# Optimization experiments

Hardware: AMD Instinct MI355X
Metric: run time of the kernel (lower is better)

## Reference

```python
import jax, jax.numpy as jnp
import numpy as np

DIM, HEADS = 768, 12
HEAD_DIM = DIM // HEADS
SCALE = HEAD_DIM ** -0.5


def setup_inputs() -> dict:
    key = jax.random.key(0)
    ks = jax.random.split(key, 16)
    B, LQ, LK = 8, 512, 512
    s = DIM ** -0.5
    inp = {
        "query": jax.random.normal(ks[0], (B, LQ, DIM), jnp.float32),
        "key_value": jax.random.normal(ks[1], (B, LK, DIM), jnp.float32),
        "query_coords": jax.random.normal(ks[2], (LQ, 2), jnp.float32),
        "key_coords": jax.random.normal(ks[3], (LK, 2), jnp.float32),
        "Wq": jax.random.normal(ks[4], (DIM, DIM), jnp.float32) * s,
        "bq": jnp.zeros((DIM,), jnp.float32),
        "Wk": jax.random.normal(ks[5], (DIM, DIM), jnp.float32) * s,
        "bk": jnp.zeros((DIM,), jnp.float32),
        "Wv": jax.random.normal(ks[6], (DIM, DIM), jnp.float32) * s,
        "bv": jnp.zeros((DIM,), jnp.float32),
        "Wo": jax.random.normal(ks[7], (DIM, DIM), jnp.float32) * s,
        "bo": jnp.zeros((DIM,), jnp.float32),
        "W1": jax.random.normal(ks[8], (6, DIM), jnp.float32) * (6 ** -0.5),
        "b1": jnp.zeros((DIM,), jnp.float32),
        "W2": jax.random.normal(ks[9], (DIM, HEADS), jnp.float32) * s,
        "b2": jnp.zeros((HEADS,), jnp.float32),
    }
    return inp


def reference(query, key_value, query_coords, key_coords,
              Wq, bq, Wk, bk, Wv, bv, Wo, bo, W1, b1, W2, b2):
    B, LQ, _ = query.shape
    LK = key_value.shape[1]
    # QKV projections -> [B, L, H, Dh]
    q = (query @ Wq + bq).reshape(B, LQ, HEADS, HEAD_DIM)
    k = (key_value @ Wk + bk).reshape(B, LK, HEADS, HEAD_DIM)
    v = (key_value @ Wv + bv).reshape(B, LK, HEADS, HEAD_DIM)
    # attention logits [B, H, LQ, LK]
    logits = jnp.einsum('bqhd,bkhd->bhqk', q, k) * SCALE
    # pairwise relative bias: delta [LQ, LK, 2] -> rel [LQ, LK, 6]
    delta = query_coords[:, None, :] - key_coords[None, :, :]
    rel = jnp.concatenate([delta, jnp.abs(delta), jnp.square(delta)], axis=-1)
    hidden = jax.nn.gelu(rel @ W1 + b1, approximate=False)  # [LQ, LK, DIM]
    bias = hidden @ W2 + b2  # [LQ, LK, H]
    logits = logits + jnp.transpose(bias, (2, 0, 1))[None]  # [B,H,LQ,LK]
    weights = jax.nn.softmax(logits, axis=-1)
    out = jnp.einsum('bhqk,bkhd->bqhd', weights, v).reshape(B, LQ, DIM)
    return out @ Wo + bo
```

## Files before the change

### kernel.cpp

```cpp
#include <hip/hip_runtime.h>
#include <hip/hip_bf16.h>
#include <stdint.h>
#include <math.h>

typedef __attribute__((ext_vector_type(4))) float f32x4;
typedef _Float16 f16;
typedef __attribute__((ext_vector_type(8))) _Float16 f16x8;
typedef decltype(__builtin_amdgcn_cvt_pkrtz(0.f, 0.f)) pk16;

#define DIM   768
#define NH    12
#define HD    64
#define NB    8
#define SEQ   512
#define SCALE 0.125f

#define GN    161
#define GPTS  (GN * GN)

#define MFMA16H __builtin_amdgcn_mfma_f32_16x16x32_f16

struct PrepArgs {
    const float* query; const float* key_value; f16* Xq; f16* Xkv;
    const float* W[4]; f16* WT[4];
    const float* W1; const float* b1; const float* W2;
    f16* W1tab; f16* W2tab; float* gtab32;
};

__global__ void __launch_bounds__(256) k_prep(PrepArgs pa) {
    __shared__ float tt[32][33];
    int g = blockIdx.x, t = threadIdx.x;
    if (g < 3072) {
        const float* in = (g < 1536) ? pa.query : pa.key_value;
        f16* out = (g < 1536) ? pa.Xq : pa.Xkv;
        int i = (g % 1536) * 256 + t;
        const float4* s = reinterpret_cast<const float4*>(in + i * 8);
        float4 f0 = s[0], f1 = s[1];
        union { pk16 h[4]; uint4 v; } o;
        o.h[0] = __builtin_amdgcn_cvt_pkrtz(f0.x, f0.y);
        o.h[1] = __builtin_amdgcn_cvt_pkrtz(f0.z, f0.w);
        o.h[2] = __builtin_amdgcn_cvt_pkrtz(f1.x, f1.y);
        o.h[3] = __builtin_amdgcn_cvt_pkrtz(f1.z, f1.w);
        reinterpret_cast<uint4*>(out)[i] = o.v;
    } else if (g < 5376) {
        int bi = g - 3072;
        int z = bi / 576, rem = bi % 576;
        int bx = rem % 24, by = rem / 24;
        const float* W = pa.W[z];
        f16* WT = pa.WT[z];
        int n0 = bx * 32, k0 = by * 32;
        int tx = t & 31, ty = t >> 5;
#pragma unroll
        for (int j = 0; j < 4; ++j)
            tt[ty + 8 * j][tx] = W[(k0 + ty + 8 * j) * DIM + n0 + tx];
        __syncthreads();
#pragma unroll
        for (int j = 0; j < 4; ++j)
            WT[(n0 + ty + 8 * j) * DIM + k0 + tx] = (f16)tt[tx][ty + 8 * j];
    } else {
        int i = (g - 5376) * 256 + t;
        if (i < 3072) {
            int lane = i & 63;
            int hi = lane >> 4, m = lane & 15;
            int u = (i >> 6) * 16 + m;
#pragma unroll
            for (int e = 0; e < 8; ++e) {
                float v = 0.f;
                if (hi == 0) {
                    if (e < 6) v = pa.W1[e * DIM + u];
                    else if (e == 6) v = pa.b1[u];
                }
                pa.W1tab[i * 8 + e] = (f16)v;
            }
        } else if (i < 4608) {
            int i2 = i - 3072;
            int j = i2 >> 6, lane = i2 & 63;
            int gq = lane >> 4, h = lane & 15;
#pragma unroll
            for (int e = 0; e < 8; ++e) {
                int u = 32 * j + ((e >> 2) << 4) + (gq << 2) + (e & 3);
                float v = (h < 12) ? pa.W2[u * 12 + h] : 0.f;
                pa.W2tab[i2 * 8 + e] = (f16)v;
            }
        } else {
            int i2 = i - 4608;
            float x = (i2 + 0.5f) * (1.0f / 256.0f) - 8.0f;
            pa.gtab32[i2] = 0.5f * x * (1.0f + erff(x * 0.70710678f));
        }
    }
}

__global__ void __launch_bounds__(256) k_grid(const f16x8* __restrict__ W1tab,
                                              const f16x8* __restrict__ W2tab,
                                              const float* __restrict__ b2,
                                              const float* __restrict__ gtab32,
                                              f16* __restrict__ grid16) {
    __shared__ float tab[4096];
    int t = threadIdx.x, lane = t & 63, w = t >> 6;
    {
        const uint4* gt = (const uint4*)gtab32;
        uint4* st = (uint4*)tab;
#pragma unroll
        for (int i = 0; i < 4; ++i) st[i * 256 + t] = gt[i * 256 + t];
    }
    int hi = lane >> 4, m = lane & 15;
    int p0 = blockIdx.x * 64 + w * 16;
    int p = p0 + m;
    int gy = p / GN, gx = p - gy * GN;
    float dx = gx * 0.125f - 10.0f;
    float dy = gy * 0.125f - 10.0f;

    union { f16x8 v; pk16 h2[4]; } rf;
    { f16x8 zz = {}; rf.v = zz; }
    if (hi == 0) {
        rf.h2[0] = __builtin_amdgcn_cvt_pkrtz(dx, dy);
        rf.h2[1] = __builtin_amdgcn_cvt_pkrtz(fabsf(dx), fabsf(dy));
        rf.h2[2] = __builtin_amdgcn_cvt_pkrtz(dx * dx, dy * dy);
        rf.h2[3] = __builtin_amdgcn_cvt_pkrtz(1.0f, 0.0f);
    }

    float b2h = (m < 12) ? b2[m] : 0.f;
    f32x4 acc = {b2h, b2h, b2h, b2h};
    const f32x4 zero = {};
    const f16x8* w1p = W1tab + lane;
    const f16x8* w2p = W2tab + lane;
    __syncthreads();

#pragma unroll 2
    for (int j = 0; j < 24; ++j) {
        f16x8 a0  = w1p[(2 * j) * 64];
        f16x8 a1  = w1p[(2 * j + 1) * 64];
        f16x8 w2v = w2p[j * 64];
        f32x4 pre0 = MFMA16H(a0, rf.v, zero, 0, 0, 0);
        f32x4 pre1 = MFMA16H(a1, rf.v, zero, 0, 0, 0);
        float s0[4], s1[4];
#pragma unroll
        for (int e = 0; e < 4; ++e) {
            float x0 = pre0[e];
            float xi0 = __builtin_amdgcn_fmed3f(__builtin_fmaf(x0, 256.f, 2048.f), 0.f, 4095.f);
            float g0 = tab[(int)xi0];
            s0[e] = (x0 > 8.f) ? x0 : g0;
            float x1 = pre1[e];
            float xi1 = __builtin_amdgcn_fmed3f(__builtin_fmaf(x1, 256.f, 2048.f), 0.f, 4095.f);
            float g1 = tab[(int)xi1];
            s1[e] = (x1 > 8.f) ? x1 : g1;
        }
        union { f16x8 v; pk16 h2[4]; } pav;
        pav.h2[0] = __builtin_amdgcn_cvt_pkrtz(s0[0], s0[1]);
        pav.h2[1] = __builtin_amdgcn_cvt_pkrtz(s0[2], s0[3]);
        pav.h2[2] = __builtin_amdgcn_cvt_pkrtz(s1[0], s1[1]);
        pav.h2[3] = __builtin_amdgcn_cvt_pkrtz(s1[2], s1[3]);
        acc = MFMA16H(pav.v, w2v, acc, 0, 0, 0);
    }
    if (m < 12) {
#pragma unroll
        for (int r = 0; r < 4; ++r) {
            int pr = p0 + hi * 4 + r;
            if (pr < GPTS) grid16[pr * 16 + m] = (f16)acc[r];
        }
    }
}

struct MQArgs {
    const float* qc; const float* kc;
    const f16* grid16; f16* bias16;
    const f16* Xq; const f16* Xkv;
    const f16* WqT; const f16* WkT; const f16* WvT;
    const float* bq; const float* bk; const float* bv;
    f16* q_ws; f16* k_ws; f16* v_t;
};

__global__ void __launch_bounds__(256) k_mq5(MQArgs a) {
    __shared__ uint4 lds[1024];
    int bid = blockIdx.x, t = threadIdx.x;
    int lane = t & 63, w = t >> 6;
    int hi = lane >> 4, lm = lane & 15;
    int xcd = bid & 7, slot = bid >> 3;

    if (slot >= 16) {
        int lid = xcd * 288 + (slot - 16);
        int m_group = lid / 36;
        int within = lid - m_group * 36;
        int z = within / 12;
        int n_tile = within - z * 12;
        int m0 = m_group * 64, n0 = n_tile * 64;
        const f16* X = (z == 0) ? a.Xq : a.Xkv;
        const f16* Wt = (z == 0) ? a.WqT : (z == 1) ? a.WkT : a.WvT;
        const float* bias = (z == 0) ? a.bq : (z == 1) ? a.bk : a.bv;
        f16* out = (z == 0) ? a.q_ws : (z == 1) ? a.k_ws : a.v_t;

        int wr = w >> 1, wc = w & 1;
        int srow = t >> 2, sslot = t & 3;
        const f16* Ag = X + (m0 + srow) * DIM + sslot * 8;
        const f16* Bg = Wt + (n0 + srow) * DIM + sslot * 8;
        int wi = srow * 4 + (sslot ^ ((srow >> 1) & 3));

        int aidx[2], bidx[2];
#pragma unroll
        for (int i = 0; i < 2; ++i) {
            int ar = wr * 32 + i * 16 + lm;
            aidx[i] = ar * 4 + (hi ^ ((ar >> 1) & 3));
            int br = wc * 32 + i * 16 + lm;
            bidx[i] = 256 + br * 4 + (hi ^ ((br >> 1) & 3));
        }

        f32x4 acc[2][2] = {};
        {
            uint4 a0 = *(const uint4*)(Ag);
            uint4 b0 = *(const uint4*)(Bg);
            lds[wi] = a0;
            lds[256 + wi] = b0;
        }
        uint4 sA1 = *(const uint4*)(Ag + 32);
        uint4 sB1 = *(const uint4*)(Bg + 32);
        uint4 sA0 = *(const uint4*)(Ag + 64);
        uint4 sB0 = *(const uint4*)(Bg + 64);
        __syncthreads();

#define MQ_COMPUTE(kt)                                                        \
        {                                                                     \
            int bo = ((kt) & 1) << 9;                                         \
            f16x8 af0 = *(const f16x8*)&lds[bo + aidx[0]];                    \
            f16x8 af1 = *(const f16x8*)&lds[bo + aidx[1]];                    \
            f16x8 bf0 = *(const f16x8*)&lds[bo + bidx[0]];                    \
            f16x8 bf1 = *(const f16x8*)&lds[bo + bidx[1]];                    \
            acc[0][0] = MFMA16H(af0, bf0, acc[0][0], 0, 0, 0);                \
            acc[0][1] = MFMA16H(af0, bf1, acc[0][1], 0, 0, 0);                \
            acc[1][0] = MFMA16H(af1, bf0, acc[1][0], 0, 0, 0);                \
            acc[1][1] = MFMA16H(af1, bf1, acc[1][1], 0, 0, 0);                \
        }

        for (int kp = 0; kp < 12; ++kp) {
            int kt = 2 * kp;
            MQ_COMPUTE(kt)
            {
                int bo2 = (((kt) & 1) << 9) ^ 512;
                lds[bo2 + wi] = sA1;
                lds[bo2 + 256 + wi] = sB1;
                if (kt + 3 < 24) {
                    sA1 = *(const uint4*)(Ag + (kt + 3) * 32);
                    sB1 = *(const uint4*)(Bg + (kt + 3) * 32);
                }
                __syncthreads();
            }
            kt = 2 * kp + 1;
            MQ_COMPUTE(kt)
            if (kt < 23) {
                int bo2 = (((kt) & 1) << 9) ^ 512;
                lds[bo2 + wi] = sA0;
                lds[bo2 + 256 + wi] = sB0;
                if (kt + 3 < 24) {
                    sA0 = *(const uint4*)(Ag + (kt + 3) * 32);
                    sB0 = *(const uint4*)(Bg + (kt + 3) * 32);
                }
                __syncthreads();
            }
        }
#undef MQ_COMPUTE

#pragma unroll
        for (int mi = 0; mi < 2; ++mi)
#pragma unroll
            for (int ni = 0; ni < 2; ++ni) {
                int n = n0 + wc * 32 + ni * 16 + lm;
                float bn = bias[n];
                int h = n >> 6, d = n & 63;
                int mbase = m0 + wr * 32 + mi * 16 + hi * 4;
                int bb = mbase >> 9, l0 = mbase & 511;
                if (z == 2) {
                    union { pk16 h2[2]; uint2 u2; } o;
                    o.h2[0] = __builtin_amdgcn_cvt_pkrtz(acc[mi][ni][0] + bn, acc[mi][ni][1] + bn);
                    o.h2[1] = __builtin_amdgcn_cvt_pkrtz(acc[mi][ni][2] + bn, acc[mi][ni][3] + bn);
                    *reinterpret_cast<uint2*>(out + (((bb * NH + h) * HD) + d) * SEQ + l0) = o.u2;
                } else {
#pragma unroll
                    for (int r = 0; r < 4; ++r)
                        out[(((bb * NH + h) * SEQ) + l0 + r) * HD + d] = (f16)(acc[mi][ni][r] + bn);
                }
            }
    } else {
        int id = xcd * 16 + slot;
#pragma unroll 2
        for (int i = 0; i < 8; ++i) {
            int p = id * 2048 + i * 256 + t;
            int qi = p >> 9, ki = p & 511;
            float dx = a.qc[2 * qi] - a.kc[2 * ki];
            float dy = a.qc[2 * qi + 1] - a.kc[2 * ki + 1];
            float fxf = __builtin_amdgcn_fmed3f(__builtin_fmaf(dx, 8.f, 80.f), 0.f, 159.9999f);
            float fyf = __builtin_amdgcn_fmed3f(__builtin_fmaf(dy, 8.f, 80.f), 0.f, 159.9999f);
            int ix = (int)fxf, iy = (int)fyf;
            float fx = fxf - (float)ix, fy = fyf - (float)iy;
            const f16* c00 = a.grid16 + (iy * GN + ix) * 16;
            f16x8 g00 = *(const f16x8*)(c00);
            f16x8 g00b = *(const f16x8*)(c00 + 8);
            f16x8 g01 = *(const f16x8*)(c00 + 16);
            f16x8 g01b = *(const f16x8*)(c00 + 24);
            f16x8 g10 = *(const f16x8*)(c00 + GN * 16);
            f16x8 g10b = *(const f16x8*)(c00 + GN * 16 + 8);
            f16x8 g11 = *(const f16x8*)(c00 + GN * 16 + 16);
            f16x8 g11b = *(const f16x8*)(c00 + GN * 16 + 24);
            float o[12];
#pragma unroll
            for (int h = 0; h < 12; ++h) {
                float v00 = (float)(h < 8 ? g00[h] : g00b[h - 8]);
                float v01 = (float)(h < 8 ? g01[h] : g01b[h - 8]);
                float v10 = (float)(h < 8 ? g10[h] : g10b[h - 8]);
                float v11 = (float)(h < 8 ? g11[h] : g11b[h - 8]);
                float v0 = __builtin_fmaf(fx, v01 - v00, v00);
                float v1 = __builtin_fmaf(fx, v11 - v10, v10);
                o[h] = __builtin_fmaf(fy, v1 - v0, v0);
            }
#pragma unroll
            for (int h = 0; h < 12; ++h)
                a.bias16[h * (SEQ * SEQ) + p] = (f16)o[h];
        }
    }
}

__global__ void __launch_bounds__(256) k_gemmO2(const f16* __restrict__ X,
                                                const f16* __restrict__ WT,
                                                const float* __restrict__ bias,
                                                float* __restrict__ out) {
    __shared__ uint4 lds[1024];
    int bid = blockIdx.x, t = threadIdx.x;
    int lane = t & 63, w = t >> 6;
    int hi = lane >> 4, lm = lane & 15;
    int xcd = bid & 7, slot = bid >> 3;
    int lid = xcd * 96 + slot;
    int m_group = lid / 12, n_tile = lid % 12;
    int m0 = m_group * 64, n0 = n_tile * 64;

    int wr = w >> 1, wc = w & 1;
    int srow = t >> 2, sslot = t & 3;
    const f16* Ag = X + (m0 + srow) * DIM + sslot * 8;
    const f16* Bg = WT + (n0 + srow) * DIM + sslot * 8;
    int wi = srow * 4 + (sslot ^ ((srow >> 1) & 3));

    int aidx[2], bidx[2];
#pragma unroll
    for (int i = 0; i < 2; ++i) {
        int ar = wr * 32 + i * 16 + lm;
        aidx[i] = ar * 4 + (hi ^ ((ar >> 1) & 3));
        int br = wc * 32 + i * 16 + lm;
        bidx[i] = 256 + br * 4 + (hi ^ ((br >> 1) & 3));
    }

    f32x4 acc[2][2] = {};
    {
        uint4 a0 = *(const uint4*)(Ag);
        uint4 b0 = *(const uint4*)(Bg);
        lds[wi] = a0;
        lds[256 + wi] = b0;
    }
    uint4 sA1 = *(const uint4*)(Ag + 32);
    uint4 sB1 = *(const uint4*)(Bg + 32);
    uint4 sA0 = *(const uint4*)(Ag + 64);
    uint4 sB0 = *(const uint4*)(Bg + 64);
    __syncthreads();

#define GO_COMPUTE(kt)                                                        \
    {                                                                         \
        int bo = ((kt) & 1) << 9;                                             \
        f16x8 af0 = *(const f16x8*)&lds[bo + aidx[0]];                        \
        f16x8 af1 = *(const f16x8*)&lds[bo + aidx[1]];                        \
        f16x8 bf0 = *(const f16x8*)&lds[bo + bidx[0]];                        \
        f16x8 bf1 = *(const f16x8*)&lds[bo + bidx[1]];                        \
        acc[0][0] = MFMA16H(af0, bf0, acc[0][0], 0, 0, 0);                    \
        acc[0][1] = MFMA16H(af0, bf1, acc[0][1], 0, 0, 0);                    \
        acc[1][0] = MFMA16H(af1, bf0, acc[1][0], 0, 0, 0);                    \
        acc[1][1] = MFMA16H(af1, bf1, acc[1][1], 0, 0, 0);                    \
    }

    for (int kp = 0; kp < 12; ++kp) {
        int kt = 2 * kp;
        GO_COMPUTE(kt)
        {
            int bo2 = (((kt) & 1) << 9) ^ 512;
            lds[bo2 + wi] = sA1;
            lds[bo2 + 256 + wi] = sB1;
            if (kt + 3 < 24) {
                sA1 = *(const uint4*)(Ag + (kt + 3) * 32);
                sB1 = *(const uint4*)(Bg + (kt + 3) * 32);
            }
            __syncthreads();
        }
        kt = 2 * kp + 1;
        GO_COMPUTE(kt)
        if (kt < 23) {
            int bo2 = (((kt) & 1) << 9) ^ 512;
            lds[bo2 + wi] = sA0;
            lds[bo2 + 256 + wi] = sB0;
            if (kt + 3 < 24) {
                sA0 = *(const uint4*)(Ag + (kt + 3) * 32);
                sB0 = *(const uint4*)(Bg + (kt + 3) * 32);
            }
            __syncthreads();
        }
    }
#undef GO_COMPUTE

#pragma unroll
    for (int mi = 0; mi < 2; ++mi)
#pragma unroll
        for (int ni = 0; ni < 2; ++ni) {
            int n = n0 + wc * 32 + ni * 16 + lm;
            float bn = bias[n];
#pragma unroll
            for (int r = 0; r < 4; ++r) {
                int m = m0 + wr * 32 + mi * 16 + hi * 4 + r;
                out[m * DIM + n] = acc[mi][ni][r] + bn;
            }
        }
}

__global__ void __launch_bounds__(256) k_attn4(const f16* __restrict__ q_ws,
                                               const f16* __restrict__ k_ws,
                                               const f16* __restrict__ v_t,
                                               const f16* __restrict__ bias16,
                                               f16* __restrict__ attn_out) {
    __shared__ __align__(16) unsigned short sm16[32 * 520];
    __shared__ float inv32[32];
    int bid = blockIdx.x;
    int xcd = bid & 7, slot = bid >> 3;
    int g = xcd * 12 + (slot >> 4);
    int h = g % 12, b = g / 12;
    int qt = slot & 15;
    int q0 = qt * 32;
    int t = threadIdx.x, lane = t & 63, w = t >> 6;
    int lrow = lane & 15, hi = lane >> 4;
    int bh = b * NH + h;
    const f16* Q = q_ws + (bh * SEQ + q0) * HD;
    const f16* K = k_ws + bh * SEQ * HD;
    const f16* Bias = bias16 + (h * SEQ + q0) * SEQ;

    f16x8 aq[2][2];
#pragma unroll
    for (int rt = 0; rt < 2; ++rt)
#pragma unroll
        for (int ds = 0; ds < 2; ++ds) {
            f16x8 v = *(const f16x8*)(Q + (rt * 16 + lrow) * HD + ds * 32 + hi * 8);
            aq[rt][ds] = v * (f16)SCALE;
        }

#pragma unroll
    for (int ct = 0; ct < 8; ++ct) {
        f32x4 acc0 = {}, acc1 = {};
        int kk = w * 128 + ct * 16 + lrow;
#pragma unroll
        for (int ds = 0; ds < 2; ++ds) {
            f16x8 bk = *(const f16x8*)(K + kk * HD + ds * 32 + hi * 8);
            acc0 = MFMA16H(aq[0][ds], bk, acc0, 0, 0, 0);
            acc1 = MFMA16H(aq[1][ds], bk, acc1, 0, 0, 0);
        }
#pragma unroll
        for (int r = 0; r < 4; ++r) {
            int row0 = hi * 4 + r;
            sm16[row0 * 520 + kk] = (unsigned short)__builtin_bit_cast(unsigned short,
                (f16)(acc0[r] + (float)Bias[row0 * SEQ + kk]));
            int row1 = 16 + hi * 4 + r;
            sm16[row1 * 520 + kk] = (unsigned short)__builtin_bit_cast(unsigned short,
                (f16)(acc1[r] + (float)Bias[row1 * SEQ + kk]));
        }
    }
    __syncthreads();

    {
        int row = t >> 3, seg = t & 7;
        int base = row * 520 + 2 * seg;
        float mx = -1e30f;
#pragma unroll 8
        for (int j = 0; j < 32; ++j) {
            union { uint u; f16 h[2]; } cv;
            cv.u = *(const uint*)&sm16[base + 16 * j];
            mx = fmaxf(mx, fmaxf((float)cv.h[0], (float)cv.h[1]));
        }
        mx = fmaxf(mx, __shfl_xor(mx, 1));
        mx = fmaxf(mx, __shfl_xor(mx, 2));
        mx = fmaxf(mx, __shfl_xor(mx, 4));
        float s = 0.f;
#pragma unroll 8
        for (int j = 0; j < 32; ++j) {
            union { uint u; f16 h[2]; } cv;
            cv.u = *(const uint*)&sm16[base + 16 * j];
            float p0 = __builtin_amdgcn_exp2f(((float)cv.h[0] - mx) * 1.442695041f);
            float p1 = __builtin_amdgcn_exp2f(((float)cv.h[1] - mx) * 1.442695041f);
            s += p0 + p1;
            union { pk16 h; uint u; } o;
            o.h = __builtin_amdgcn_cvt_pkrtz(p0, p1);
            *(uint*)&sm16[base + 16 * j] = o.u;
        }
        s += __shfl_xor(s, 1);
        s += __shfl_xor(s, 2);
        s += __shfl_xor(s, 4);
        if (seg == 0) inv32[row] = 1.0f / s;
    }
    __syncthreads();

    const f16* Vt = v_t + bh * HD * SEQ + (w * 16 + lrow) * SEQ;
    f32x4 oacc0 = {}, oacc1 = {};
    for (int kt = 0; kt < 16; ++kt) {
        f16x8 bv = *(const f16x8*)(Vt + kt * 32 + hi * 8);
        f16x8 pa0 = *(const f16x8*)&sm16[lrow * 520 + kt * 32 + hi * 8];
        f16x8 pa1 = *(const f16x8*)&sm16[(16 + lrow) * 520 + kt * 32 + hi * 8];
        oacc0 = MFMA16H(pa0, bv, oacc0, 0, 0, 0);
        oacc1 = MFMA16H(pa1, bv, oacc1, 0, 0, 0);
    }
#pragma unroll
    for (int r = 0; r < 4; ++r) {
        int row0 = hi * 4 + r;
        float v0 = oacc0[r] * inv32[row0];
        attn_out[(b * SEQ + q0 + row0) * DIM + h * HD + w * 16 + lrow] = (f16)v0;
        int row1 = 16 + hi * 4 + r;
        float v1 = oacc1[r] * inv32[row1];
        attn_out[(b * SEQ + q0 + row1) * DIM + h * HD + w * 16 + lrow] = (f16)v1;
    }
}

extern "C" void kernel_launch(void* const* d_in, const int* in_sizes, int n_in,
                              void* d_out, int out_size, void* d_ws, size_t ws_size,
                              hipStream_t stream) {
    const float* query     = (const float*)d_in[0];
    const float* key_value = (const float*)d_in[1];
    const float* qc        = (const float*)d_in[2];
    const float* kc        = (const float*)d_in[3];
    const float* Wq        = (const float*)d_in[4];
    const float* bq        = (const float*)d_in[5];
    const float* Wk        = (const float*)d_in[6];
    const float* bk        = (const float*)d_in[7];
    const float* Wv        = (const float*)d_in[8];
    const float* bv        = (const float*)d_in[9];
    const float* Wo        = (const float*)d_in[10];
    const float* bo        = (const float*)d_in[11];
    const float* W1        = (const float*)d_in[12];
    const float* b1        = (const float*)d_in[13];
    const float* W2        = (const float*)d_in[14];
    const float* b2        = (const float*)d_in[15];

    char* ws = (char*)d_ws;
    f16* Xq   = (f16*)(ws + 0);
    f16* Xkv  = (f16*)(ws + 6291456);
    f16* WqT  = (f16*)(ws + 12582912);
    f16* WkT  = (f16*)(ws + 13762560);
    f16* WvT  = (f16*)(ws + 14942208);
    f16* WoT  = (f16*)(ws + 16121856);
    f16* q_ws = (f16*)(ws + 17301504);
    f16* k_ws = (f16*)(ws + 23592960);
    f16* v_t  = (f16*)(ws + 29884416);
    f16* bias16   = (f16*)(ws + 36175872);
    f16* W1tab    = (f16*)(ws + 42467328);
    f16* W2tab    = (f16*)(ws + 42516480);
    float* gtab32 = (float*)(ws + 42541056);
    f16* grid16   = (f16*)(ws + 42557440);
    f16* attn_out = Xq;

    PrepArgs pa;
    pa.query = query; pa.key_value = key_value; pa.Xq = Xq; pa.Xkv = Xkv;
    pa.W[0] = Wq; pa.W[1] = Wk; pa.W[2] = Wv; pa.W[3] = Wo;
    pa.WT[0] = WqT; pa.WT[1] = WkT; pa.WT[2] = WvT; pa.WT[3] = WoT;
    pa.W1 = W1; pa.b1 = b1; pa.W2 = W2;
    pa.W1tab = W1tab; pa.W2tab = W2tab; pa.gtab32 = gtab32;
    k_prep<<<dim3(5410), dim3(256), 0, stream>>>(pa);

    k_grid<<<dim3(406), dim3(256), 0, stream>>>((const f16x8*)W1tab, (const f16x8*)W2tab,
                                                b2, gtab32, grid16);

    MQArgs mq;
    mq.qc = qc; mq.kc = kc;
    mq.grid16 = grid16; mq.bias16 = bias16;
    mq.Xq = Xq; mq.Xkv = Xkv;
    mq.WqT = WqT; mq.WkT = WkT; mq.WvT = WvT;
    mq.bq = bq; mq.bk = bk; mq.bv = bv;
    mq.q_ws = q_ws; mq.k_ws = k_ws; mq.v_t = v_t;
    k_mq5<<<dim3(2432), dim3(256), 0, stream>>>(mq);

    k_attn4<<<dim3(1536), dim3(256), 0, stream>>>(q_ws, k_ws, v_t, bias16, attn_out);
    k_gemmO2<<<dim3(768), dim3(256), 0, stream>>>(attn_out, WoT, bo, (float*)d_out);
}
```

Before: 106.6 us.

## Fuse Q projection into attention kernel, drop Q from projection GEMM

Moves the Q projection out of the combined QKV GEMM kernel and computes each 32x64 Q tile inside the attention block from Xq and WqT, using a double-buffered LDS loop. This removes the q_ws write and read round trip and shrinks the projection launch. The cost is that each attention block now runs a 24-step K-loop GEMM with small tiles and a barrier per step before attention starts, which adds latency and reloads the WqT head slice in every block. attn_out moves to the old q_ws buffer so it no longer aliases Xq, which the attention blocks now read.

```diff
diff --git a/kernel.cpp b/kernel.cpp
--- a/kernel.cpp
+++ b/kernel.cpp
@@ -164,13 +164,13 @@
 struct MQArgs {
     const float* qc; const float* kc;
     const f16* grid16; f16* bias16;
-    const f16* Xq; const f16* Xkv;
-    const f16* WqT; const f16* WkT; const f16* WvT;
-    const float* bq; const float* bk; const float* bv;
-    f16* q_ws; f16* k_ws; f16* v_t;
+    const f16* Xkv;
+    const f16* WkT; const f16* WvT;
+    const float* bk; const float* bv;
+    f16* k_ws; f16* v_t;
 };
 
-__global__ void __launch_bounds__(256) k_mq5(MQArgs a) {
+__global__ void __launch_bounds__(256) k_mq7(MQArgs a) {
     __shared__ uint4 lds[1024];
     int bid = blockIdx.x, t = threadIdx.x;
     int lane = t & 63, w = t >> 6;
@@ -178,16 +178,16 @@
     int xcd = bid & 7, slot = bid >> 3;
 
     if (slot >= 16) {
-        int lid = xcd * 288 + (slot - 16);
-        int m_group = lid / 36;
-        int within = lid - m_group * 36;
+        int lid = xcd * 192 + (slot - 16);
+        int m_group = lid / 24;
+        int within = lid - m_group * 24;
         int z = within / 12;
         int n_tile = within - z * 12;
         int m0 = m_group * 64, n0 = n_tile * 64;
-        const f16* X = (z == 0) ? a.Xq : a.Xkv;
-        const f16* Wt = (z == 0) ? a.WqT : (z == 1) ? a.WkT : a.WvT;
-        const float* bias = (z == 0) ? a.bq : (z == 1) ? a.bk : a.bv;
-        f16* out = (z == 0) ? a.q_ws : (z == 1) ? a.k_ws : a.v_t;
+        const f16* X = a.Xkv;
+        const f16* Wt = (z == 0) ? a.WkT : a.WvT;
+        const float* bias = (z == 0) ? a.bk : a.bv;
+        f16* out = (z == 0) ? a.k_ws : a.v_t;
 
         int wr = w >> 1, wc = w & 1;
         int srow = t >> 2, sslot = t & 3;
@@ -267,7 +267,7 @@
                 int h = n >> 6, d = n & 63;
                 int mbase = m0 + wr * 32 + mi * 16 + hi * 4;
                 int bb = mbase >> 9, l0 = mbase & 511;
-                if (z == 2) {
+                if (z == 1) {
                     union { pk16 h2[2]; uint2 u2; } o;
                     o.h2[0] = __builtin_amdgcn_cvt_pkrtz(acc[mi][ni][0] + bn, acc[mi][ni][1] + bn);
                     o.h2[1] = __builtin_amdgcn_cvt_pkrtz(acc[mi][ni][2] + bn, acc[mi][ni][3] + bn);
@@ -413,13 +413,19 @@
         }
 }
 
-__global__ void __launch_bounds__(256) k_attn4(const f16* __restrict__ q_ws,
+__global__ void __launch_bounds__(256) k_attn6(const f16* __restrict__ Xq,
+                                               const f16* __restrict__ WqT,
+                                               const float* __restrict__ bq,
                                                const f16* __restrict__ k_ws,
                                                const f16* __restrict__ v_t,
                                                const f16* __restrict__ bias16,
                                                f16* __restrict__ attn_out) {
-    __shared__ __align__(16) unsigned short sm16[32 * 520];
-    __shared__ float inv32[32];
+    __shared__ __align__(16) char smem[33408];
+    unsigned short* sm16 = (unsigned short*)smem;
+    float* inv32 = (float*)(smem + 33280);
+    uint4* dbuf = (uint4*)smem;
+    f16* qlds = (f16*)(smem + 12288);
+
     int bid = blockIdx.x;
     int xcd = bid & 7, slot = bid >> 3;
     int g = xcd * 12 + (slot >> 4);
@@ -429,18 +435,74 @@
     int t = threadIdx.x, lane = t & 63, w = t >> 6;
     int lrow = lane & 15, hi = lane >> 4;
     int bh = b * NH + h;
-    const f16* Q = q_ws + (bh * SEQ + q0) * HD;
+
+    {
+        const f16* Ag = Xq + (b * SEQ + q0) * DIM;
+        const f16* Bg = WqT + (h * HD) * DIM;
+        int arow = t >> 2, aslot = t & 3;
+        int awi = arow * 4 + (aslot ^ ((arow >> 1) & 3));
+        int bwi = 128 + arow * 4 + (aslot ^ ((arow >> 1) & 3));
+        int wr2 = w >> 1, wc2 = w & 1;
+        int ar = wr2 * 16 + lrow;
+        int qa_idx = ar * 4 + (hi ^ ((ar >> 1) & 3));
+        int qb_idx[2];
+#pragma unroll
+        for (int i = 0; i < 2; ++i) {
+            int br = wc2 * 32 + i * 16 + lrow;
+            qb_idx[i] = 128 + br * 4 + (hi ^ ((br >> 1) & 3));
+        }
+
+        f32x4 qacc[2] = {};
+        if (t < 128) dbuf[awi] = *(const uint4*)(Ag + arow * DIM + aslot * 8);
+        dbuf[bwi] = *(const uint4*)(Bg + arow * DIM + aslot * 8);
+        __syncthreads();
+
+        for (int kt = 0; kt < 24; ++kt) {
+            uint4 na, nb;
+            bool pf = kt < 23;
+            if (pf) {
+                if (t < 128) na = *(const uint4*)(Ag + arow * DIM + (kt + 1) * 32 + aslot * 8);
+                nb = *(const uint4*)(Bg + arow * DIM + (kt + 1) * 32 + aslot * 8);
+            }
+            int bo = (kt & 1) * 384;
+            f16x8 qaf = *(const f16x8*)&dbuf[bo + qa_idx];
+            f16x8 qbf0 = *(const f16x8*)&dbuf[bo + qb_idx[0]];
+            f16x8 qbf1 = *(const f16x8*)&dbuf[bo + qb_idx[1]];
+            qacc[0] = MFMA16H(qaf, qbf0, qacc[0], 0, 0, 0);
+            qacc[1] = MFMA16H(qaf, qbf1, qacc[1], 0, 0, 0);
+            if (pf) {
+                int bo2 = bo ^ 384;
+                if (t < 128) dbuf[bo2 + awi] = na;
+                dbuf[bo2 + bwi] = nb;
+                __syncthreads();
+            }
+        }
+        __syncthreads();
+#pragma unroll
+        for (int i = 0; i < 2; ++i) {
+            int col = wc2 * 32 + i * 16 + lrow;
+            float bn = bq[h * HD + col];
+#pragma unroll
+            for (int r = 0; r < 4; ++r) {
+                int row = wr2 * 16 + hi * 4 + r;
+                qlds[row * 72 + col] = (f16)(qacc[i][r] + bn);
+            }
+        }
+    }
+    __syncthreads();
+
+    f16x8 aq[2][2];
+#pragma unroll
+    for (int rt = 0; rt < 2; ++rt)
+#pragma unroll
+        for (int ds = 0; ds < 2; ++ds) {
+            f16x8 v = *(const f16x8*)&qlds[(rt * 16 + lrow) * 72 + ds * 32 + hi * 8];
+            aq[rt][ds] = v * (f16)SCALE;
+        }
+    __syncthreads();
+
     const f16* K = k_ws + bh * SEQ * HD;
     const f16* Bias = bias16 + (h * SEQ + q0) * SEQ;
-
-    f16x8 aq[2][2];
-#pragma unroll
-    for (int rt = 0; rt < 2; ++rt)
-#pragma unroll
-        for (int ds = 0; ds < 2; ++ds) {
-            f16x8 v = *(const f16x8*)(Q + (rt * 16 + lrow) * HD + ds * 32 + hi * 8);
-            aq[rt][ds] = v * (f16)SCALE;
-        }
 
 #pragma unroll
     for (int ct = 0; ct < 8; ++ct) {
@@ -470,9 +532,9 @@
         float mx = -1e30f;
 #pragma unroll 8
         for (int j = 0; j < 32; ++j) {
-            union { uint u; f16 h[2]; } cv;
+            union { uint u; f16 hh[2]; } cv;
             cv.u = *(const uint*)&sm16[base + 16 * j];
-            mx = fmaxf(mx, fmaxf((float)cv.h[0], (float)cv.h[1]));
+            mx = fmaxf(mx, fmaxf((float)cv.hh[0], (float)cv.hh[1]));
         }
         mx = fmaxf(mx, __shfl_xor(mx, 1));
         mx = fmaxf(mx, __shfl_xor(mx, 2));
@@ -480,13 +542,13 @@
         float s = 0.f;
 #pragma unroll 8
         for (int j = 0; j < 32; ++j) {
-            union { uint u; f16 h[2]; } cv;
+            union { uint u; f16 hh[2]; } cv;
             cv.u = *(const uint*)&sm16[base + 16 * j];
-            float p0 = __builtin_amdgcn_exp2f(((float)cv.h[0] - mx) * 1.442695041f);
-            float p1 = __builtin_amdgcn_exp2f(((float)cv.h[1] - mx) * 1.442695041f);
+            float p0 = __builtin_amdgcn_exp2f(((float)cv.hh[0] - mx) * 1.442695041f);
+            float p1 = __builtin_amdgcn_exp2f(((float)cv.hh[1] - mx) * 1.442695041f);
             s += p0 + p1;
-            union { pk16 h; uint u; } o;
-            o.h = __builtin_amdgcn_cvt_pkrtz(p0, p1);
+            union { pk16 hh; uint u; } o;
+            o.hh = __builtin_amdgcn_cvt_pkrtz(p0, p1);
             *(uint*)&sm16[base + 16 * j] = o.u;
         }
         s += __shfl_xor(s, 1);
@@ -543,7 +605,7 @@
     f16* WkT  = (f16*)(ws + 13762560);
     f16* WvT  = (f16*)(ws + 14942208);
     f16* WoT  = (f16*)(ws + 16121856);
-    f16* q_ws = (f16*)(ws + 17301504);
+    f16* attn_out = (f16*)(ws + 17301504);
     f16* k_ws = (f16*)(ws + 23592960);
     f16* v_t  = (f16*)(ws + 29884416);
     f16* bias16   = (f16*)(ws + 36175872);
@@ -551,7 +613,6 @@
     f16* W2tab    = (f16*)(ws + 42516480);
     float* gtab32 = (float*)(ws + 42541056);
     f16* grid16   = (f16*)(ws + 42557440);
-    f16* attn_out = Xq;
 
     PrepArgs pa;
     pa.query = query; pa.key_value = key_value; pa.Xq = Xq; pa.Xkv = Xkv;
@@ -567,12 +628,12 @@
     MQArgs mq;
     mq.qc = qc; mq.kc = kc;
     mq.grid16 = grid16; mq.bias16 = bias16;
-    mq.Xq = Xq; mq.Xkv = Xkv;
-    mq.WqT = WqT; mq.WkT = WkT; mq.WvT = WvT;
-    mq.bq = bq; mq.bk = bk; mq.bv = bv;
-    mq.q_ws = q_ws; mq.k_ws = k_ws; mq.v_t = v_t;
-    k_mq5<<<dim3(2432), dim3(256), 0, stream>>>(mq);
-
-    k_attn4<<<dim3(1536), dim3(256), 0, stream>>>(q_ws, k_ws, v_t, bias16, attn_out);
+    mq.Xkv = Xkv;
+    mq.WkT = WkT; mq.WvT = WvT;
+    mq.bk = bk; mq.bv = bv;
+    mq.k_ws = k_ws; mq.v_t = v_t;
+    k_mq7<<<dim3(1664), dim3(256), 0, stream>>>(mq);
+
+    k_attn6<<<dim3(1536), dim3(256), 0, stream>>>(Xq, WqT, bq, k_ws, v_t, bias16, attn_out);
     k_gemmO2<<<dim3(768), dim3(256), 0, stream>>>(attn_out, WoT, bo, (float*)d_out);
 }
```

Result: no change. 107.5 us (+0.8%).
